# Kernel tuning notes

Hardware: AMD Instinct MI355X
Metric: run time of the kernel (lower is better)

The kernel has to match this reference:

```python
import jax, jax.numpy as jnp
import numpy as np

B, L, D, H = 8, 4096, 1024, 16
HD = D // H
HID = 4096  # int(D * 4.0)
KSZ = 25    # moving-average kernel size
EPS = 1e-6


def _layernorm(x, w, b):
    mu = jnp.mean(x, axis=-1, keepdims=True)
    var = jnp.mean((x - mu) ** 2, axis=-1, keepdims=True)
    return (x - mu) / jnp.sqrt(var + EPS) * w + b


def _lin(x, W, b):
    # eqx.nn.Linear stores weight as (out, in)
    return jnp.einsum('...i,oi->...o', x, W) + b


def setup_inputs() -> dict:
    key = jax.random.key(0)
    ks = jax.random.split(key, 8)
    s = 0.02
    return {
        'x': jax.random.normal(ks[0], (B, L, D), dtype=jnp.float32),
        'ln1_w': jnp.ones((D,), jnp.float32),
        'ln1_b': jnp.zeros((D,), jnp.float32),
        'Wq': jax.random.normal(ks[1], (D, D), jnp.float32) * s,
        'bq': jnp.zeros((D,), jnp.float32),
        'Wk': jax.random.normal(ks[2], (D, D), jnp.float32) * s,
        'bk': jnp.zeros((D,), jnp.float32),
        'Wv': jax.random.normal(ks[3], (D, D), jnp.float32) * s,
        'bv': jnp.zeros((D,), jnp.float32),
        'Wo': jax.random.normal(ks[4], (D, D), jnp.float32) * s,
        'bo': jnp.zeros((D,), jnp.float32),
        'ln2_w': jnp.ones((D,), jnp.float32),
        'ln2_b': jnp.zeros((D,), jnp.float32),
        'W1': jax.random.normal(ks[5], (HID, D), jnp.float32) * s,
        'b1': jnp.zeros((HID,), jnp.float32),
        'W2': jax.random.normal(ks[6], (D, HID), jnp.float32) * s,
        'b2': jnp.zeros((D,), jnp.float32),
    }


def reference(x, ln1_w, ln1_b, Wq, bq, Wk, bk, Wv, bv, Wo, bo,
              ln2_w, ln2_b, W1, b1, W2, b2):
    b, l, d = x.shape
    # --- AutoCorrelation attention on norm1(x) ---
    y = _layernorm(x, ln1_w, ln1_b)
    Q = _lin(y, Wq, bq).reshape(b, l, H, HD).transpose(0, 2, 1, 3)  # (B,H,L,hd)
    K = _lin(y, Wk, bk).reshape(b, l, H, HD).transpose(0, 2, 1, 3)
    V = _lin(y, Wv, bv).reshape(b, l, H, HD).transpose(0, 2, 1, 3)
    qf = jnp.fft.rfft(Q, axis=2)
    kf = jnp.fft.rfft(K, axis=2)
    corr_time = jnp.fft.irfft(qf * jnp.conjugate(kf), n=l, axis=2)  # (B,H,L,hd)
    corr = jnp.mean(corr_time, axis=-1)                             # (B,H,L)
    attn = jax.nn.softmax(corr, axis=-1)
    out = jnp.einsum('bhl,bhld->bhd', attn, V)                      # (B,H,hd)
    # faithful lossy reshape: transpose(0,2,1) -> (B,hd,H), flatten to (B,D)
    out = out.transpose(0, 2, 1).reshape(b, d)
    out = _lin(out, Wo, bo)
    y = jnp.broadcast_to(out[:, None, :], (b, l, d))  # repeat over L
    x = x + y
    # --- Series decomposition: depthwise moving average, subtract trend ---
    kern = jnp.ones((KSZ, 1, d), x.dtype) / KSZ
    xt = x.transpose(0, 2, 1)  # (B,D,L)
    trend = jax.lax.conv_general_dilated(
        xt, kern, window_strides=(1,), padding='SAME',
        dimension_numbers=('NCL', 'LIO', 'NCL'), feature_group_count=d)
    x = x - trend.transpose(0, 2, 1)
    # --- MLP (dropout p=0 -> identity) ---
    y = _layernorm(x, ln2_w, ln2_b)
    y = _lin(jax.nn.gelu(_lin(y, W1, b1)), W2, b2)
    return x + y
```

## Files before the change

kernel.cpp:

```cpp
#include <hip/hip_runtime.h>

#define DEV __device__ __forceinline__

typedef __attribute__((ext_vector_type(8))) short bf16x8;
typedef __attribute__((ext_vector_type(4))) float f32x4;
typedef unsigned short u16;
typedef __attribute__((address_space(1))) const void* gvp;
typedef __attribute__((address_space(3))) void* svp;

DEV u16 f2bf(float f){
  unsigned u = __float_as_uint(f);
  u = (u + 0x7FFFu + ((u >> 16) & 1u)) >> 16;
  return (u16)u;
}
DEV float bf2f(u16 v){ return __uint_as_float(((unsigned)v) << 16); }
DEV float2 cmul(float2 a, float2 b){ return make_float2(a.x*b.x - a.y*b.y, a.x*b.y + a.y*b.x); }
DEV int rev8(int i){
  return ((i & 7) << 9) | ((i & 0x38) << 3) | ((i & 0x1C0) >> 3) | ((i >> 9) & 7);
}

__global__ void k_cvt(const float* __restrict__ s, u16* __restrict__ d, int n){
  int i = blockIdx.x * 256 + threadIdx.x;
  if (i < n) d[i] = f2bf(s[i]);
}

__global__ void k_cat2(const float* __restrict__ a, const float* __restrict__ b, float* __restrict__ o){
  int i = blockIdx.x * 256 + threadIdx.x;
  if (i < 1024){ o[i] = a[i]; o[1024 + i] = b[i]; }
}

__global__ void k_twinit(float2* __restrict__ tw){
  int k = blockIdx.x * 256 + threadIdx.x;
  if (k < 2048){
    float sn, cs;
    sincosf(-1.5339807878856412e-03f * (float)k, &sn, &cs);
    tw[k] = make_float2(cs, sn);
  }
}

__global__ __launch_bounds__(256) void k_ln(const float* __restrict__ x, const float* __restrict__ w,
                                            const float* __restrict__ b, u16* __restrict__ y){
  const int row = blockIdx.x;
  const int tid = threadIdx.x;
  const float4 v = ((const float4*)(x + (size_t)row * 1024))[tid];
  float s1 = v.x + v.y + v.z + v.w;
  float s2 = v.x*v.x + v.y*v.y + v.z*v.z + v.w*v.w;
  #pragma unroll
  for (int o = 32; o > 0; o >>= 1){ s1 += __shfl_down(s1, o); s2 += __shfl_down(s2, o); }
  __shared__ float r1[4], r2[4];
  __shared__ float mu_s, rs_s;
  const int wv = tid >> 6;
  if ((tid & 63) == 0){ r1[wv] = s1; r2[wv] = s2; }
  __syncthreads();
  if (tid == 0){
    float t1 = r1[0]+r1[1]+r1[2]+r1[3], t2 = r2[0]+r2[1]+r2[2]+r2[3];
    float mu = t1 * (1.0f/1024.0f);
    float var = t2 * (1.0f/1024.0f) - mu*mu;
    mu_s = mu; rs_s = rsqrtf(var + 1e-6f);
  }
  __syncthreads();
  const float mu = mu_s, rs = rs_s;
  const float4 wv4 = ((const float4*)w)[tid];
  const float4 bv4 = ((const float4*)b)[tid];
  ushort4 o4;
  o4.x = f2bf((v.x-mu)*rs*wv4.x + bv4.x);
  o4.y = f2bf((v.y-mu)*rs*wv4.y + bv4.y);
  o4.z = f2bf((v.z-mu)*rs*wv4.z + bv4.z);
  o4.w = f2bf((v.w-mu)*rs*wv4.w + bv4.w);
  ((ushort4*)(y + (size_t)row*1024))[tid] = o4;
}

template<int MODE>
__launch_bounds__(512, 2)
__global__ void k_gemm5(const u16* __restrict__ A, const u16* __restrict__ Bw,
                        const float* __restrict__ bias, void* __restrict__ out, void* __restrict__ out2,
                        int M, int N, int K)
{
  __shared__ __align__(16) u16 SMEM[65536];
  u16 (*LA)[16384] = reinterpret_cast<u16(*)[16384]>(SMEM);
  u16 (*LB)[16384] = reinterpret_cast<u16(*)[16384]>(SMEM + 32768);
  const int tid = threadIdx.x;
  const int wave = tid >> 6, lane = tid & 63;
  const int l15 = lane & 15, l4 = lane >> 4;
  const int wrq = wave >> 2, wcq = wave & 3;
  (void)M;

  const int nwg = gridDim.x;
  const int q8 = nwg >> 3;
  const int wg = (blockIdx.x & 7) * q8 + (blockIdx.x >> 3);
  const int NBN = N >> 8;
  const int bm = wg / NBN, bn = wg % NBN;
  const int NT = K >> 6, NI = NT >> 1;

  const int sr8 = lane >> 3;
  const int sch8 = ((lane & 7) ^ (sr8 & 7)) * 8;
  const u16* gA = A  + ((size_t)(bm*256 + wave*16 + sr8)) * K + sch8;
  const u16* gB = Bw + ((size_t)(bn*256 + wave*16 + sr8)) * K + sch8;
  const size_t gH = (size_t)128 * K;
  const size_t gJ = (size_t)8 * K;
  const int lbase = wave * 1024;

  const unsigned swzb = (unsigned)((l4 ^ (l15 & 7)) * 16);
  const unsigned uA0  = (unsigned)(uintptr_t)&LA[0][0] + (unsigned)((wrq*64 + l15)*128) + swzb;
  const unsigned uB0  = (unsigned)(uintptr_t)&LB[0][0] + (unsigned)((wcq*32 + l15)*128) + swzb;
  const unsigned uA0x = uA0 ^ 64u, uB0x = uB0 ^ 64u;
  const unsigned uA1  = uA0 + 32768u, uA1x = uA0x + 32768u;
  const unsigned uB1  = uB0 + 32768u, uB1x = uB0x + 32768u;

  f32x4 acc[8][4];
  const f32x4 z4 = {0.f, 0.f, 0.f, 0.f};
  #pragma unroll
  for (int m = 0; m < 8; ++m)
    #pragma unroll
    for (int n = 0; n < 4; ++n) acc[m][n] = z4;

#define DSR(dst, base, OFF) asm volatile("ds_read_b128 %0, %1 offset:" #OFF : "=v"(dst) : "v"(base))

#define LDA_Q0(b0, b1) do{ \
  DSR(fa[0], b0, 0);    DSR(fa[1], b1, 0); \
  DSR(fa[2], b0, 2048); DSR(fa[3], b1, 2048); \
  DSR(fa[4], b0, 4096); DSR(fa[5], b1, 4096); \
  DSR(fa[6], b0, 6144); DSR(fa[7], b1, 6144); }while(0)
#define LDA_Q1(b0, b1) do{ \
  DSR(fa[0], b0, 16384); DSR(fa[1], b1, 16384); \
  DSR(fa[2], b0, 18432); DSR(fa[3], b1, 18432); \
  DSR(fa[4], b0, 20480); DSR(fa[5], b1, 20480); \
  DSR(fa[6], b0, 22528); DSR(fa[7], b1, 22528); }while(0)
#define LDB_Q0(dst, b0, b1) do{ \
  DSR(dst[0], b0, 0);    DSR(dst[1], b1, 0); \
  DSR(dst[2], b0, 2048); DSR(dst[3], b1, 2048); }while(0)
#define LDB_Q1(dst, b0, b1) do{ \
  DSR(dst[0], b0, 16384); DSR(dst[1], b1, 16384); \
  DSR(dst[2], b0, 18432); DSR(dst[3], b1, 18432); }while(0)

#define STG(LD, G, DB, HALF, TK) do{ \
    const int tk_ = (TK) < NT ? (TK) : NT - 1; \
    const u16* g_ = (G) + (size_t)tk_ * 64 + (size_t)(HALF) * gH; \
    u16* l_ = &LD[DB][lbase + (HALF) * 8192]; \
    __builtin_amdgcn_global_load_lds((gvp)g_,        (svp)l_,        16, 0, 0); \
    __builtin_amdgcn_global_load_lds((gvp)(g_ + gJ), (svp)(l_ + 512),16, 0, 0); \
  }while(0)

#define MFMA16(QA, QB, FB) do{ \
    __builtin_amdgcn_s_setprio(1); \
    _Pragma("unroll") for (int kk = 0; kk < 2; ++kk) \
    _Pragma("unroll") for (int mm = 0; mm < 4; ++mm) \
    _Pragma("unroll") for (int nn = 0; nn < 2; ++nn) \
      acc[(QA)*4+mm][(QB)*2+nn] = __builtin_amdgcn_mfma_f32_16x16x32_bf16( \
          fa[mm*2+kk], FB[nn*2+kk], acc[(QA)*4+mm][(QB)*2+nn], 0, 0, 0); \
    __builtin_amdgcn_s_setprio(0); \
  }while(0)

#define SBAR  __builtin_amdgcn_s_barrier()
#define SB0   __builtin_amdgcn_sched_barrier(0)
#define LGKM0 do{ asm volatile("s_waitcnt lgkmcnt(0)" ::: "memory"); SB0; }while(0)
#define LGKM8 asm volatile("s_waitcnt lgkmcnt(8)" ::: "memory")
#define VM4   asm volatile("s_waitcnt vmcnt(4)" ::: "memory")

  STG(LA, gA, 0, 0, 0); STG(LA, gA, 0, 1, 0);
  STG(LB, gB, 0, 0, 0); STG(LB, gB, 0, 1, 0);
  STG(LA, gA, 1, 0, 1);
  STG(LB, gB, 1, 1, 1);
  VM4; SBAR;

  for (int it = 0; it < NI; ++it){
    const int u = 2 * it;
    bf16x8 fa[8], fbA[4], fbB[4];
    LDB_Q0(fbA, uB0, uB0x);
    LDA_Q0(uA0, uA0x);
    STG(LA, gA, 1, 1, u+1); STG(LB, gB, 1, 0, u+1);
    LGKM8;
    SBAR; LGKM0; MFMA16(0, 0, fbA); SB0; SBAR;
    LDB_Q1(fbB, uB0, uB0x);
    SBAR; LGKM0; MFMA16(0, 1, fbB); SB0; SBAR;
    LDA_Q1(uA0, uA0x);
    STG(LA, gA, 0, 0, u+2);
    SBAR; LGKM0; MFMA16(1, 1, fbB); SB0; SBAR;
    STG(LB, gB, 0, 1, u+2);
    VM4; SBAR; SB0; MFMA16(1, 0, fbA); SB0; SBAR;
    LDB_Q0(fbA, uB1, uB1x);
    LDA_Q0(uA1, uA1x);
    STG(LA, gA, 0, 1, u+2); STG(LB, gB, 0, 0, u+2);
    LGKM8;
    SBAR; LGKM0; MFMA16(0, 0, fbA); SB0; SBAR;
    LDB_Q1(fbB, uB1, uB1x);
    SBAR; LGKM0; MFMA16(0, 1, fbB); SB0; SBAR;
    LDA_Q1(uA1, uA1x);
    STG(LA, gA, 1, 0, u+3);
    SBAR; LGKM0; MFMA16(1, 1, fbB); SB0; SBAR;
    STG(LB, gB, 1, 1, u+3);
    VM4; SBAR; SB0; MFMA16(1, 0, fbA); SB0; SBAR;
  }
#undef DSR
#undef LDA_Q0
#undef LDA_Q1
#undef LDB_Q0
#undef LDB_Q1
#undef STG
#undef MFMA16
#undef SBAR
#undef SB0
#undef LGKM0
#undef LGKM8
#undef VM4

  if (MODE == 3){
    asm volatile("s_waitcnt vmcnt(0)" ::: "memory");
    __syncthreads();
    u16* T = SMEM;
    const int bq = bm >> 4;
    const int l0 = (bm & 15) * 256;
    u16* dstb = (u16*)(bn < 4 ? out : out2) + ((size_t)bq*1024 + (bn & 3)*256)*4096 + l0;
    #pragma unroll
    for (int half = 0; half < 2; ++half){
      #pragma unroll
      for (int nn = 0; nn < 2; ++nn){
        const int n = half*2 + nn;
        const int colh = wcq*32 + nn*16 + l15;
        const float bv = bias[bn*256 + half*128 + colh];
        #pragma unroll
        for (int m = 0; m < 8; ++m){
          const int lrow = (m>>2)*128 + wrq*64 + (m&3)*16 + l4*4;
          ushort4 o4;
          o4.x = f2bf(acc[m][n][0] + bv);
          o4.y = f2bf(acc[m][n][1] + bv);
          o4.z = f2bf(acc[m][n][2] + bv);
          o4.w = f2bf(acc[m][n][3] + bv);
          *(ushort4*)&T[colh*264 + lrow] = o4;
        }
      }
      __syncthreads();
      {
        const int c = tid >> 2, lch = (tid & 3) * 64;
        u16* drow = dstb + (size_t)(half*128 + c) * 4096 + lch;
        const u16* srow = &T[c*264 + lch];
        #pragma unroll
        for (int i = 0; i < 8; ++i)
          *(bf16x8*)(drow + i*8) = *(const bf16x8*)(srow + i*8);
      }
      __syncthreads();
    }
  } else {
    #pragma unroll
    for (int m = 0; m < 8; ++m){
      const int gr0 = bm*256 + (m>>2)*128 + wrq*64 + (m&3)*16 + l4*4;
      #pragma unroll
      for (int n = 0; n < 4; ++n){
        const int gc = bn*256 + (n>>1)*128 + wcq*32 + (n&1)*16 + l15;
        const float bv = bias[gc];
        #pragma unroll
        for (int r2 = 0; r2 < 4; ++r2){
          const size_t off = (size_t)(gr0 + r2) * N + gc;
          float v = acc[m][n][r2] + bv;
          if (MODE == 1){
            const float a = 0.7978845608028654f * (v + 0.044715f * v * v * v);
            const float e = __expf(2.0f * a);
            const float th = (e - 1.0f) / (e + 1.0f);
            ((u16*)out)[off] = f2bf(0.5f * v * (1.0f + th));
          } else {
            float* op = (float*)out;
            op[off] += v;
          }
        }
      }
    }
  }
}

DEV void fft4096_dif8(float2* Z, const float2* tw, int tid){
  const float C = 0.70710678118654752f;
  #pragma unroll
  for (int s = 4; s >= 1; --s){
    const int q = 1 << (3*(s-1));
    const int step = 1 << (12 - 3*s);
    #pragma unroll
    for (int tt = tid; tt < 512; tt += 256){
      const int j = tt & (q-1);
      const int base = ((tt >> (3*(s-1))) << (3*s)) + j;
      float2 a0 = Z[base],       a1 = Z[base+q],   a2 = Z[base+2*q], a3 = Z[base+3*q];
      float2 a4 = Z[base+4*q],   a5 = Z[base+5*q], a6 = Z[base+6*q], a7 = Z[base+7*q];
      float2 e0 = {a0.x+a4.x, a0.y+a4.y}, o0 = {a0.x-a4.x, a0.y-a4.y};
      float2 e1 = {a2.x+a6.x, a2.y+a6.y}, o1 = {a2.x-a6.x, a2.y-a6.y};
      float2 e2 = {a1.x+a5.x, a1.y+a5.y}, o2 = {a1.x-a5.x, a1.y-a5.y};
      float2 e3 = {a3.x+a7.x, a3.y+a7.y}, o3 = {a3.x-a7.x, a3.y-a7.y};
      float2 E0 = {e0.x+e1.x, e0.y+e1.y}, E1 = {e0.x-e1.x, e0.y-e1.y};
      float2 E2 = {e2.x+e3.x, e2.y+e3.y}, E3 = {e2.x-e3.x, e2.y-e3.y};
      float2 u0 = {E0.x+E2.x, E0.y+E2.y};
      float2 u4 = {E0.x-E2.x, E0.y-E2.y};
      float2 njE3 = {E3.y, -E3.x};
      float2 u2 = {E1.x+njE3.x, E1.y+njE3.y};
      float2 u6 = {E1.x-njE3.x, E1.y-njE3.y};
      float2 W1o2 = {C*(o2.x+o2.y), C*(o2.y-o2.x)};
      float2 W3o2 = {C*(o2.y-o2.x), -C*(o2.x+o2.y)};
      float2 W1o3 = {C*(o3.x+o3.y), C*(o3.y-o3.x)};
      float2 W3o3 = {C*(o3.y-o3.x), -C*(o3.x+o3.y)};
      float2 njo1 = {o1.y, -o1.x};
      float2 u1 = {o0.x + W1o2.x + njo1.x + W3o3.x, o0.y + W1o2.y + njo1.y + W3o3.y};
      float2 u3 = {o0.x + W3o2.x - njo1.x + W1o3.x, o0.y + W3o2.y - njo1.y + W1o3.y};
      float2 u5 = {o0.x - W1o2.x + njo1.x - W3o3.x, o0.y - W1o2.y + njo1.y - W3o3.y};
      float2 u7 = {o0.x - W3o2.x - njo1.x - W1o3.x, o0.y - W3o2.y - njo1.y - W1o3.y};
      const float2 w1 = tw[j*step];
      const float2 w2 = tw[2*j*step];
      const float2 w4 = tw[4*j*step];
      const float2 w3 = cmul(w1, w2);
      const float2 w5 = cmul(w1, w4);
      const float2 w6 = cmul(w2, w4);
      const float2 w7 = cmul(w3, w4);
      Z[base]     = u0;
      Z[base+q]   = cmul(u1, w1);
      Z[base+2*q] = cmul(u2, w2);
      Z[base+3*q] = cmul(u3, w3);
      Z[base+4*q] = cmul(u4, w4);
      Z[base+5*q] = cmul(u5, w5);
      Z[base+6*q] = cmul(u6, w6);
      Z[base+7*q] = cmul(u7, w7);
    }
    __syncthreads();
  }
}

DEV void fft4096_dit8_inv(float2* Z, const float2* tw, int tid){
  const float C = 0.70710678118654752f;
  #pragma unroll
  for (int s = 1; s <= 4; ++s){
    const int q = 1 << (3*(s-1));
    const int step = 1 << (12 - 3*s);
    #pragma unroll
    for (int tt = tid; tt < 512; tt += 256){
      const int j = tt & (q-1);
      const int base = ((tt >> (3*(s-1))) << (3*s)) + j;
      float2 a0 = Z[base],       a1 = Z[base+q],   a2 = Z[base+2*q], a3 = Z[base+3*q];
      float2 a4 = Z[base+4*q],   a5 = Z[base+5*q], a6 = Z[base+6*q], a7 = Z[base+7*q];
      float2 w1 = tw[j*step];   w1.y = -w1.y;
      float2 w2 = tw[2*j*step]; w2.y = -w2.y;
      float2 w4 = tw[4*j*step]; w4.y = -w4.y;
      const float2 w3 = cmul(w1, w2);
      const float2 w5 = cmul(w1, w4);
      const float2 w6 = cmul(w2, w4);
      const float2 w7 = cmul(w3, w4);
      a1 = cmul(a1, w1); a2 = cmul(a2, w2); a3 = cmul(a3, w3);
      a4 = cmul(a4, w4); a5 = cmul(a5, w5); a6 = cmul(a6, w6); a7 = cmul(a7, w7);
      float2 e0 = {a0.x+a4.x, a0.y+a4.y}, o0 = {a0.x-a4.x, a0.y-a4.y};
      float2 e1 = {a2.x+a6.x, a2.y+a6.y}, o1 = {a2.x-a6.x, a2.y-a6.y};
      float2 e2 = {a1.x+a5.x, a1.y+a5.y}, o2 = {a1.x-a5.x, a1.y-a5.y};
      float2 e3 = {a3.x+a7.x, a3.y+a7.y}, o3 = {a3.x-a7.x, a3.y-a7.y};
      float2 E0 = {e0.x+e1.x, e0.y+e1.y}, E1 = {e0.x-e1.x, e0.y-e1.y};
      float2 E2 = {e2.x+e3.x, e2.y+e3.y}, E3 = {e2.x-e3.x, e2.y-e3.y};
      float2 pjE3 = {-E3.y, E3.x};
      float2 W1o2 = {C*(o2.x-o2.y), C*(o2.x+o2.y)};
      float2 W3o2 = {-C*(o2.x+o2.y), C*(o2.x-o2.y)};
      float2 W1o3 = {C*(o3.x-o3.y), C*(o3.x+o3.y)};
      float2 W3o3 = {-C*(o3.x+o3.y), C*(o3.x-o3.y)};
      float2 pjo1 = {-o1.y, o1.x};
      Z[base]     = make_float2(E0.x+E2.x, E0.y+E2.y);
      Z[base+q]   = make_float2(o0.x + W1o2.x + pjo1.x + W3o3.x, o0.y + W1o2.y + pjo1.y + W3o3.y);
      Z[base+2*q] = make_float2(E1.x+pjE3.x, E1.y+pjE3.y);
      Z[base+3*q] = make_float2(o0.x + W3o2.x - pjo1.x + W1o3.x, o0.y + W3o2.y - pjo1.y + W1o3.y);
      Z[base+4*q] = make_float2(E0.x-E2.x, E0.y-E2.y);
      Z[base+5*q] = make_float2(o0.x - W1o2.x + pjo1.x - W3o3.x, o0.y - W1o2.y + pjo1.y - W3o3.y);
      Z[base+6*q] = make_float2(E1.x-pjE3.x, E1.y-pjE3.y);
      Z[base+7*q] = make_float2(o0.x - W3o2.x - pjo1.x - W1o3.x, o0.y - W3o2.y - pjo1.y - W1o3.y);
    }
    __syncthreads();
  }
}

__global__ __launch_bounds__(256) void k_fftcorr(const u16* __restrict__ Qt, const u16* __restrict__ Kt,
                                                 const float2* __restrict__ twg, float* __restrict__ S){
  __shared__ float2 Z[4096];
  __shared__ float2 tw[2048];
  const int tid = threadIdx.x;
  const int bh = blockIdx.x, dg = blockIdx.y;
  for (int k = tid; k < 2048; k += 256) tw[k] = twg[k];
  float2 sa[16];
  #pragma unroll
  for (int j = 0; j < 16; ++j) sa[j] = make_float2(0.f, 0.f);
  __syncthreads();
  for (int dd = 0; dd < 8; ++dd){
    const int d = dg*8 + dd;
    const u16* q  = Qt + ((size_t)bh*64 + d) * 4096;
    const u16* kp = Kt + ((size_t)bh*64 + d) * 4096;
    for (int i = tid; i < 4096; i += 256)
      Z[i] = make_float2(bf2f(q[i]), bf2f(kp[i]));
    __syncthreads();
    fft4096_dif8(Z, tw, tid);
    #pragma unroll
    for (int j = 0; j < 16; ++j){
      const int p = j*256 + tid;
      const int f = rev8(p);
      const int p2 = rev8((4096 - f) & 4095);
      const float2 a = Z[p];
      const float2 c = Z[p2];
      const float qr = 0.5f * (a.x + c.x);
      const float qi = 0.5f * (a.y - c.y);
      const float kr = 0.5f * (a.y + c.y);
      const float ki = 0.5f * (c.x - a.x);
      sa[j].x += qr*kr + qi*ki;
      sa[j].y += qi*kr - qr*ki;
    }
    __syncthreads();
  }
  float* Sg = S + (size_t)bh * 8192;
  #pragma unroll
  for (int j = 0; j < 16; ++j){
    const int p = j*256 + tid;
    atomicAdd(&Sg[2*p + 0], sa[j].x);
    atomicAdd(&Sg[2*p + 1], sa[j].y);
  }
}

__global__ __launch_bounds__(256) void k_isoftmax(const float* __restrict__ S, const float2* __restrict__ twg,
                                                  float* __restrict__ attn){
  __shared__ float2 Z[4096];
  __shared__ float2 tw[2048];
  __shared__ float red[4];
  __shared__ float bc;
  const int tid = threadIdx.x;
  const int bh = blockIdx.x;
  for (int k = tid; k < 2048; k += 256) tw[k] = twg[k];
  const float2* Sg = (const float2*)(S + (size_t)bh * 8192);
  for (int i = tid; i < 4096; i += 256) Z[i] = Sg[i];
  __syncthreads();
  fft4096_dit8_inv(Z, tw, tid);
  const float scale = 1.0f / (4096.0f * 64.0f);
  float cr[16];
  float lmax = -1e30f;
  #pragma unroll
  for (int j = 0; j < 16; ++j){
    const float c = Z[j*256 + tid].x * scale;
    cr[j] = c;
    lmax = fmaxf(lmax, c);
  }
  #pragma unroll
  for (int o = 32; o > 0; o >>= 1) lmax = fmaxf(lmax, __shfl_down(lmax, o));
  if ((tid & 63) == 0) red[tid >> 6] = lmax;
  __syncthreads();
  if (tid == 0) bc = fmaxf(fmaxf(red[0], red[1]), fmaxf(red[2], red[3]));
  __syncthreads();
  const float gmax = bc;
  float lsum = 0.f;
  #pragma unroll
  for (int j = 0; j < 16; ++j){ cr[j] = __expf(cr[j] - gmax); lsum += cr[j]; }
  #pragma unroll
  for (int o = 32; o > 0; o >>= 1) lsum += __shfl_down(lsum, o);
  if ((tid & 63) == 0) red[tid >> 6] = lsum;
  __syncthreads();
  if (tid == 0) bc = red[0] + red[1] + red[2] + red[3];
  __syncthreads();
  const float inv = 1.0f / bc;
  float* at = attn + (size_t)bh * 4096;
  #pragma unroll
  for (int j = 0; j < 16; ++j) at[j*256 + tid] = cr[j] * inv;
}

__global__ __launch_bounds__(256) void k_yw(const float* __restrict__ attn, const u16* __restrict__ Y,
                                            float* __restrict__ yw){
  __shared__ float at[128*20 + 4];
  const int b = blockIdx.x, lq = blockIdx.y;
  const int l0 = lq * 128;
  const int tid = threadIdx.x;
  for (int idx = tid; idx < 2048; idx += 256){
    const int h = idx >> 7, l = idx & 127;
    at[l*20 + h] = attn[((size_t)b*16 + h)*4096 + l0 + l];
  }
  __syncthreads();
  float acc[16][4];
  #pragma unroll
  for (int h = 0; h < 16; ++h)
    #pragma unroll
    for (int j = 0; j < 4; ++j) acc[h][j] = 0.f;
  const u16* yb = Y + ((size_t)b*4096 + l0)*1024 + tid*4;
  for (int l = 0; l < 128; ++l){
    const ushort4 yv4 = *(const ushort4*)(yb + (size_t)l*1024);
    const float y0 = bf2f(yv4.x), y1 = bf2f(yv4.y), y2 = bf2f(yv4.z), y3 = bf2f(yv4.w);
    #pragma unroll
    for (int hq = 0; hq < 4; ++hq){
      const float4 a4 = *(const float4*)&at[l*20 + hq*4];
      acc[hq*4+0][0] += a4.x*y0; acc[hq*4+0][1] += a4.x*y1; acc[hq*4+0][2] += a4.x*y2; acc[hq*4+0][3] += a4.x*y3;
      acc[hq*4+1][0] += a4.y*y0; acc[hq*4+1][1] += a4.y*y1; acc[hq*4+1][2] += a4.y*y2; acc[hq*4+1][3] += a4.y*y3;
      acc[hq*4+2][0] += a4.z*y0; acc[hq*4+2][1] += a4.z*y1; acc[hq*4+2][2] += a4.z*y2; acc[hq*4+2][3] += a4.z*y3;
      acc[hq*4+3][0] += a4.w*y0; acc[hq*4+3][1] += a4.w*y1; acc[hq*4+3][2] += a4.w*y2; acc[hq*4+3][3] += a4.w*y3;
    }
  }
  float* ywb = yw + (size_t)b*16*1024 + tid*4;
  #pragma unroll
  for (int h = 0; h < 16; ++h)
    #pragma unroll
    for (int j = 0; j < 4; ++j)
      atomicAdd(&ywb[(size_t)h*1024 + j], acc[h][j]);
}

__global__ __launch_bounds__(256) void k_vproj(const float* __restrict__ yw, const float* __restrict__ Wv,
                                               const float* __restrict__ bv, float* __restrict__ oav){
  __shared__ float yv[1024];
  const int b = blockIdx.x, h = blockIdx.y;
  const int tid = threadIdx.x;
  for (int i = tid; i < 1024; i += 256) yv[i] = yw[((size_t)b*16 + h)*1024 + i];
  __syncthreads();
  const int hd = tid >> 2, q = tid & 3;
  const float4* wr = (const float4*)(Wv + (size_t)(h*64 + hd)*1024 + q*256);
  float acc = 0.f;
  #pragma unroll 4
  for (int i = 0; i < 64; ++i){
    const float4 w4 = wr[i];
    acc += yv[q*256+4*i]*w4.x + yv[q*256+4*i+1]*w4.y + yv[q*256+4*i+2]*w4.z + yv[q*256+4*i+3]*w4.w;
  }
  acc += __shfl_xor(acc, 1);
  acc += __shfl_xor(acc, 2);
  if (q == 0) oav[(size_t)b*1024 + hd*16 + h] = acc + bv[h*64 + hd];
}

__global__ __launch_bounds__(256) void k_proj(const float* __restrict__ oav, const float* __restrict__ Wo,
                                              const float* __restrict__ bo, float* __restrict__ proj){
  const int b = blockIdx.x;
  const int o = blockIdx.y * 256 + threadIdx.x;
  __shared__ float xin[1024];
  for (int i = threadIdx.x; i < 1024; i += 256) xin[i] = oav[(size_t)b*1024 + i];
  __syncthreads();
  float acc = bo[o];
  const float4* wr = (const float4*)(Wo + (size_t)o * 1024);
  #pragma unroll 4
  for (int i = 0; i < 256; ++i){
    const float4 w4 = wr[i];
    acc += xin[4*i]*w4.x + xin[4*i+1]*w4.y + xin[4*i+2]*w4.z + xin[4*i+3]*w4.w;
  }
  proj[(size_t)b*1024 + o] = acc;
}

__global__ __launch_bounds__(256) void k_decomp(const float* __restrict__ x, const float* __restrict__ proj,
                                                float* __restrict__ out){
  const int b = blockIdx.x, dq = blockIdx.y, lc = blockIdx.z;
  const int d = dq*256 + threadIdx.x;
  const int l0 = lc * 256;
  const float pv = proj[(size_t)b*1024 + d];
  const float* xb = x + (size_t)b*4096*1024 + d;
  float* ob = out + (size_t)b*4096*1024 + d;
  if (lc == 0){
    float wsum = 0.f, cnt = 0.f;
    for (int j = 0; j <= 11; ++j){ wsum += xb[(size_t)j*1024]; cnt += 1.f; }
    for (int l = 0; l < 256; ++l){
      wsum += xb[(size_t)(l+12)*1024]; cnt += 1.f;
      const float xc = xb[(size_t)l*1024];
      ob[(size_t)l*1024] = xc + pv - (wsum + cnt*pv)*0.04f;
      if (l >= 12){ wsum -= xb[(size_t)(l-12)*1024]; cnt -= 1.f; }
    }
  } else if (lc == 15){
    float wsum = 0.f, cnt = 0.f;
    for (int j = l0-12; j <= l0+11; ++j){ wsum += xb[(size_t)j*1024]; cnt += 1.f; }
    for (int l = l0; l < 4096; ++l){
      if (l + 12 < 4096){ wsum += xb[(size_t)(l+12)*1024]; cnt += 1.f; }
      const float xc = xb[(size_t)l*1024];
      ob[(size_t)l*1024] = xc + pv - (wsum + cnt*pv)*0.04f;
      wsum -= xb[(size_t)(l-12)*1024]; cnt -= 1.f;
    }
  } else {
    float wsum = 0.f;
    #pragma unroll
    for (int j = -12; j <= 11; ++j) wsum += xb[(size_t)(l0+j)*1024];
    #pragma unroll 4
    for (int l = l0; l < l0 + 256; ++l){
      wsum += xb[(size_t)(l+12)*1024];
      const float xc = xb[(size_t)l*1024];
      ob[(size_t)l*1024] = xc - wsum*0.04f;
      wsum -= xb[(size_t)(l-12)*1024];
    }
  }
}

extern "C" void kernel_launch(void* const* d_in, const int* in_sizes, int n_in,
                              void* d_out, int out_size, void* d_ws, size_t ws_size,
                              hipStream_t stream){
  const float* x    = (const float*)d_in[0];
  const float* ln1w = (const float*)d_in[1];
  const float* ln1b = (const float*)d_in[2];
  const float* Wq   = (const float*)d_in[3];
  const float* bq   = (const float*)d_in[4];
  const float* Wk   = (const float*)d_in[5];
  const float* bk   = (const float*)d_in[6];
  const float* Wv   = (const float*)d_in[7];
  const float* bv   = (const float*)d_in[8];
  const float* Wo   = (const float*)d_in[9];
  const float* bo   = (const float*)d_in[10];
  const float* ln2w = (const float*)d_in[11];
  const float* ln2b = (const float*)d_in[12];
  const float* W1   = (const float*)d_in[13];
  const float* b1   = (const float*)d_in[14];
  const float* W2   = (const float*)d_in[15];
  const float* b2   = (const float*)d_in[16];
  float* out = (float*)d_out;

  char* ws = (char*)d_ws;
  u16* Qt   = (u16*)(ws + 134217728);
  u16* Kt   = (u16*)(ws + 201326592);
  u16* H1   = (u16*)(ws + 0);
  u16* Y    = (u16*)(ws + 268435456);
  float* S    = (float*)(ws + 335544320);
  float2* twg = (float2*)(ws + 339738624);
  float* attn = (float*)(ws + 339755008);
  float* yw   = (float*)(ws + 341852160);
  float* oav  = (float*)(ws + 342376448);
  float* proj = (float*)(ws + 342409216);
  float* bqk  = (float*)(ws + 342441984);
  u16* Wqkb   = (u16*)(ws + 342450176);
  u16* W1b    = (u16*)(ws + 346644480);
  u16* W2b    = (u16*)(ws + 355033088);

  k_cvt<<<4096, 256, 0, stream>>>(Wq, Wqkb,           1048576);
  k_cvt<<<4096, 256, 0, stream>>>(Wk, Wqkb + 1048576, 1048576);
  k_cvt<<<16384, 256, 0, stream>>>(W1, W1b, 4194304);
  k_cvt<<<16384, 256, 0, stream>>>(W2, W2b, 4194304);
  k_cat2<<<4, 256, 0, stream>>>(bq, bk, bqk);
  k_twinit<<<8, 256, 0, stream>>>(twg);

  k_ln<<<32768, 256, 0, stream>>>(x, ln1w, ln1b, Y);

  k_gemm5<3><<<1024, 512, 0, stream>>>(Y, Wqkb, bqk, Qt, Kt, 32768, 2048, 1024);

  hipMemsetAsync(S, 0, 4194304, stream);
  k_fftcorr<<<dim3(128, 8), 256, 0, stream>>>(Qt, Kt, twg, S);
  k_isoftmax<<<128, 256, 0, stream>>>(S, twg, attn);

  hipMemsetAsync(yw, 0, 524288, stream);
  k_yw<<<dim3(8, 32), 256, 0, stream>>>(attn, Y, yw);
  k_vproj<<<dim3(8, 16), 256, 0, stream>>>(yw, Wv, bv, oav);
  k_proj<<<dim3(8, 4), 256, 0, stream>>>(oav, Wo, bo, proj);

  k_decomp<<<dim3(8, 4, 16), 256, 0, stream>>>(x, proj, out);

  k_ln<<<32768, 256, 0, stream>>>(out, ln2w, ln2b, Y);

  k_gemm5<1><<<2048, 512, 0, stream>>>(Y, W1b, b1, H1, nullptr, 32768, 4096, 1024);
  k_gemm5<2><<<512, 512, 0, stream>>>(H1, W2b, b2, out, nullptr, 32768, 1024, 4096);
}
```

Before: 1.427 ms.

## Fuse prep kernels, replace atomic spectrum accumulation, double decomp grid

Merges the four weight-conversion launches, the bias concat and the twiddle init into a single prep kernel to cut launch overhead. k_fftcorr now writes per-group partial spectra to separate slots instead of using atomicAdd, and k_isoftmax sums the 8 partials, which removes the memset and the atomic contention. k_decomp uses 128-row chunks instead of 256, doubling the grid to 1024 blocks for more parallelism at the cost of extra halo reads. S moves to the start of the workspace, aliasing H1, which is safe because H1 is written only later.

Result: faster. 1.315 ms (-7.8%).

```diff
diff --git a/kernel.cpp b/kernel.cpp
--- a/kernel.cpp
+++ b/kernel.cpp
@@ -19,22 +19,28 @@
   return ((i & 7) << 9) | ((i & 0x38) << 3) | ((i & 0x1C0) >> 3) | ((i >> 9) & 7);
 }
 
-__global__ void k_cvt(const float* __restrict__ s, u16* __restrict__ d, int n){
-  int i = blockIdx.x * 256 + threadIdx.x;
-  if (i < n) d[i] = f2bf(s[i]);
-}
-
-__global__ void k_cat2(const float* __restrict__ a, const float* __restrict__ b, float* __restrict__ o){
-  int i = blockIdx.x * 256 + threadIdx.x;
-  if (i < 1024){ o[i] = a[i]; o[1024 + i] = b[i]; }
-}
-
-__global__ void k_twinit(float2* __restrict__ tw){
-  int k = blockIdx.x * 256 + threadIdx.x;
-  if (k < 2048){
+__global__ void k_prep(const float* __restrict__ Wq, const float* __restrict__ Wk,
+                       const float* __restrict__ W1, const float* __restrict__ W2,
+                       const float* __restrict__ bq, const float* __restrict__ bk,
+                       u16* __restrict__ Wqkb, u16* __restrict__ W1b, u16* __restrict__ W2b,
+                       float* __restrict__ bqk, float2* __restrict__ twg){
+  const size_t i = (size_t)blockIdx.x * 256 + threadIdx.x;
+  if (i < 1048576){
+    Wqkb[i] = f2bf(Wq[i]);
+  } else if (i < 2097152){
+    Wqkb[i] = f2bf(Wk[i - 1048576]);
+  } else if (i < 6291456){
+    W1b[i - 2097152] = f2bf(W1[i - 2097152]);
+  } else if (i < 10485760){
+    W2b[i - 6291456] = f2bf(W2[i - 6291456]);
+  } else if (i < 10487808){
+    const int k = (int)(i - 10485760);
     float sn, cs;
     sincosf(-1.5339807878856412e-03f * (float)k, &sn, &cs);
-    tw[k] = make_float2(cs, sn);
+    twg[k] = make_float2(cs, sn);
+  } else if (i < 10488832){
+    const int k = (int)(i - 10487808);
+    bqk[k] = bq[k]; bqk[1024 + k] = bk[k];
   }
 }
 
@@ -400,13 +406,10 @@
     }
     __syncthreads();
   }
-  float* Sg = S + (size_t)bh * 8192;
-  #pragma unroll
-  for (int j = 0; j < 16; ++j){
-    const int p = j*256 + tid;
-    atomicAdd(&Sg[2*p + 0], sa[j].x);
-    atomicAdd(&Sg[2*p + 1], sa[j].y);
-  }
+  float2* Sg = (float2*)S + ((size_t)dg*128 + bh) * 4096;
+  #pragma unroll
+  for (int j = 0; j < 16; ++j)
+    Sg[j*256 + tid] = sa[j];
 }
 
 __global__ __launch_bounds__(256) void k_isoftmax(const float* __restrict__ S, const float2* __restrict__ twg,
@@ -418,8 +421,16 @@
   const int tid = threadIdx.x;
   const int bh = blockIdx.x;
   for (int k = tid; k < 2048; k += 256) tw[k] = twg[k];
-  const float2* Sg = (const float2*)(S + (size_t)bh * 8192);
-  for (int i = tid; i < 4096; i += 256) Z[i] = Sg[i];
+  const float2* S2 = (const float2*)S;
+  for (int i = tid; i < 4096; i += 256){
+    float2 acc = make_float2(0.f, 0.f);
+    #pragma unroll
+    for (int g = 0; g < 8; ++g){
+      const float2 v = S2[((size_t)g*128 + bh) * 4096 + i];
+      acc.x += v.x; acc.y += v.y;
+    }
+    Z[i] = acc;
+  }
   __syncthreads();
   fft4096_dit8_inv(Z, tw, tid);
   const float scale = 1.0f / (4096.0f * 64.0f);
@@ -531,20 +542,20 @@
                                                 float* __restrict__ out){
   const int b = blockIdx.x, dq = blockIdx.y, lc = blockIdx.z;
   const int d = dq*256 + threadIdx.x;
-  const int l0 = lc * 256;
+  const int l0 = lc * 128;
   const float pv = proj[(size_t)b*1024 + d];
   const float* xb = x + (size_t)b*4096*1024 + d;
   float* ob = out + (size_t)b*4096*1024 + d;
   if (lc == 0){
     float wsum = 0.f, cnt = 0.f;
     for (int j = 0; j <= 11; ++j){ wsum += xb[(size_t)j*1024]; cnt += 1.f; }
-    for (int l = 0; l < 256; ++l){
+    for (int l = 0; l < 128; ++l){
       wsum += xb[(size_t)(l+12)*1024]; cnt += 1.f;
       const float xc = xb[(size_t)l*1024];
       ob[(size_t)l*1024] = xc + pv - (wsum + cnt*pv)*0.04f;
       if (l >= 12){ wsum -= xb[(size_t)(l-12)*1024]; cnt -= 1.f; }
     }
-  } else if (lc == 15){
+  } else if (lc == 31){
     float wsum = 0.f, cnt = 0.f;
     for (int j = l0-12; j <= l0+11; ++j){ wsum += xb[(size_t)j*1024]; cnt += 1.f; }
     for (int l = l0; l < 4096; ++l){
@@ -558,7 +569,7 @@
     #pragma unroll
     for (int j = -12; j <= 11; ++j) wsum += xb[(size_t)(l0+j)*1024];
     #pragma unroll 4
-    for (int l = l0; l < l0 + 256; ++l){
+    for (int l = l0; l < l0 + 128; ++l){
       wsum += xb[(size_t)(l+12)*1024];
       const float xc = xb[(size_t)l*1024];
       ob[(size_t)l*1024] = xc - wsum*0.04f;
@@ -590,11 +601,11 @@
   float* out = (float*)d_out;
 
   char* ws = (char*)d_ws;
+  float* S  = (float*)(ws + 0);
   u16* Qt   = (u16*)(ws + 134217728);
   u16* Kt   = (u16*)(ws + 201326592);
   u16* H1   = (u16*)(ws + 0);
   u16* Y    = (u16*)(ws + 268435456);
-  float* S    = (float*)(ws + 335544320);
   float2* twg = (float2*)(ws + 339738624);
   float* attn = (float*)(ws + 339755008);
   float* yw   = (float*)(ws + 341852160);
@@ -605,18 +616,12 @@
   u16* W1b    = (u16*)(ws + 346644480);
   u16* W2b    = (u16*)(ws + 355033088);
 
-  k_cvt<<<4096, 256, 0, stream>>>(Wq, Wqkb,           1048576);
-  k_cvt<<<4096, 256, 0, stream>>>(Wk, Wqkb + 1048576, 1048576);
-  k_cvt<<<16384, 256, 0, stream>>>(W1, W1b, 4194304);
-  k_cvt<<<16384, 256, 0, stream>>>(W2, W2b, 4194304);
-  k_cat2<<<4, 256, 0, stream>>>(bq, bk, bqk);
-  k_twinit<<<8, 256, 0, stream>>>(twg);
+  k_prep<<<40972, 256, 0, stream>>>(Wq, Wk, W1, W2, bq, bk, Wqkb, W1b, W2b, bqk, twg);
 
   k_ln<<<32768, 256, 0, stream>>>(x, ln1w, ln1b, Y);
 
   k_gemm5<3><<<1024, 512, 0, stream>>>(Y, Wqkb, bqk, Qt, Kt, 32768, 2048, 1024);
 
-  hipMemsetAsync(S, 0, 4194304, stream);
   k_fftcorr<<<dim3(128, 8), 256, 0, stream>>>(Qt, Kt, twg, S);
   k_isoftmax<<<128, 256, 0, stream>>>(S, twg, attn);
 
@@ -625,7 +630,7 @@
   k_vproj<<<dim3(8, 16), 256, 0, stream>>>(yw, Wv, bv, oav);
   k_proj<<<dim3(8, 4), 256, 0, stream>>>(oav, Wo, bo, proj);
 
-  k_decomp<<<dim3(8, 4, 16), 256, 0, stream>>>(x, proj, out);
+  k_decomp<<<dim3(8, 4, 32), 256, 0, stream>>>(x, proj, out);
 
   k_ln<<<32768, 256, 0, stream>>>(out, ln2w, ln2b, Y);
 
```
